# Kernel optimization log

Hardware: AMD Instinct MI355X
Metric: run time of the kernel (lower is better)

## Reference

```python
import jax, jax.numpy as jnp
import numpy as np

N_NODES = 50000
N_EDGES = 800000
N_FEATS = 64
K_HOPS = 3


def setup_inputs() -> dict:
    key = jax.random.key(0)
    k1, k2, k3 = jax.random.split(key, 3)
    x = jax.random.normal(k1, (N_NODES, N_FEATS), dtype=jnp.float32)
    edge_index = jax.random.randint(k2, (2, N_EDGES), 0, N_NODES, dtype=jnp.int32)
    # SGConv linear: out_channels = 1 (hardcoded in Net)
    W = jax.random.normal(k3, (1, N_FEATS), dtype=jnp.float32) / np.sqrt(N_FEATS)
    b = jnp.zeros((1,), dtype=jnp.float32)
    return {"x": x, "edge_index": edge_index, "W": W, "b": b}


def reference(x, edge_index, W, b):
    # SGConv: X' = (D^-1/2 (A + I) D^-1/2)^K X @ W.T + b
    N = x.shape[0]
    self_loops = jnp.arange(N, dtype=edge_index.dtype)
    row = jnp.concatenate([edge_index[0], self_loops])  # source nodes (x_j)
    col = jnp.concatenate([edge_index[1], self_loops])  # destination nodes
    # gcn_norm: degree computed at destination with unit edge weights
    deg = jax.ops.segment_sum(jnp.ones(row.shape[0], x.dtype), col, num_segments=N)
    dinv = jnp.where(deg > 0, jax.lax.rsqrt(deg), jnp.zeros_like(deg))
    norm = dinv[row] * dinv[col]  # [E + N]
    # K hops of normalized sparse propagation: out[col] += norm * x[row]
    for _ in range(K_HOPS):
        x = jax.ops.segment_sum(norm[:, None] * x[row], col, num_segments=N)
    return x @ W.T + b  # [N, 1]
```

## Files before the change

kernel.cpp:

```cpp
#include <hip/hip_runtime.h>

#define N_NODES 50000
#define N_EDGES 800000
#define N_FEATS 64
#define EB4     (N_EDGES / 4)
#define NBUCK   256
#define BRANGE  196
#define CAPB    4096
#define BZT     1024
#define PRT     512
#define HOPT    1024
#define MAXREC  (BZT * 4)

struct SmemSort { unsigned buf[MAXREC]; unsigned adr[MAXREC]; };


__global__ void __launch_bounds__(BZT) k_bucketize(
    const int* __restrict__ row, const int* __restrict__ col,
    int* __restrict__ gcur, unsigned* __restrict__ recs)
{
    __shared__ SmemSort u;
    __shared__ int s_cnt[NBUCK];
    __shared__ int s_off[NBUCK];
    __shared__ int s_wsum[4];
    __shared__ int s_total;

    const int t = threadIdx.x;
    if (t < NBUCK) s_cnt[t] = 0;
    __syncthreads();

    const int g = blockIdx.x * BZT + t;
    const bool valid = g < EB4;
    int4 c4, r4;
    int bk[4], rk[4];
    if (valid) {
        c4 = ((const int4*)col)[g];
        r4 = ((const int4*)row)[g];
        bk[0] = c4.x / BRANGE; rk[0] = atomicAdd(&s_cnt[bk[0]], 1);
        bk[1] = c4.y / BRANGE; rk[1] = atomicAdd(&s_cnt[bk[1]], 1);
        bk[2] = c4.z / BRANGE; rk[2] = atomicAdd(&s_cnt[bk[2]], 1);
        bk[3] = c4.w / BRANGE; rk[3] = atomicAdd(&s_cnt[bk[3]], 1);
    }
    __syncthreads();

    if (t < NBUCK) {
        const int lane = t & 63;
        const int cnt = s_cnt[t];
        int val = cnt;
        #pragma unroll
        for (int d = 1; d < 64; d <<= 1) {
            int tmp = __shfl_up(val, d);
            if (lane >= d) val += tmp;
        }
        if (lane == 63) s_wsum[t >> 6] = val;
        s_off[t] = val - cnt;
    }
    __syncthreads();
    if (t < NBUCK) {
        const int w4 = t >> 6;
        int base = 0;
        #pragma unroll
        for (int i = 0; i < 3; i++) if (i < w4) base += s_wsum[i];
        s_off[t] += base;
        const int cnt = s_cnt[t];
        s_cnt[t] = cnt ? atomicAdd(&gcur[t], cnt) : 0;
        if (t == 0) s_total = s_wsum[0] + s_wsum[1] + s_wsum[2] + s_wsum[3];
    }
    __syncthreads();

    if (valid) {
        const int cc[4] = {c4.x, c4.y, c4.z, c4.w};
        const int rr[4] = {r4.x, r4.y, r4.z, r4.w};
        #pragma unroll
        for (int i = 0; i < 4; i++) {
            const int b = bk[i];
            const int p = s_off[b] + rk[i];
            const int slot = s_cnt[b] + rk[i];
            u.buf[p] = ((unsigned)(cc[i] - b * BRANGE) << 16) | (unsigned)rr[i];
            u.adr[p] = (slot < CAPB) ? (unsigned)(b * CAPB + slot) : 0xFFFFFFFFu;
        }
    }
    __syncthreads();

    const int total = s_total;
    for (int p = t; p < total; p += BZT) {
        const unsigned a = u.adr[p];
        if (a != 0xFFFFFFFFu) recs[a] = u.buf[p];
    }
}

__global__ void __launch_bounds__(PRT) k_prep(
    const int* __restrict__ gcur, unsigned* __restrict__ recs,
    const float* __restrict__ x, const float* __restrict__ w,
    float* __restrict__ dinv, float* __restrict__ z0)
{
    __shared__ unsigned s_sorted[CAPB];
    __shared__ int s_deg[NBUCK];
    __shared__ int s_base[NBUCK];
    __shared__ int s_wsum[4];

    const int t = threadIdx.x;
    const int blk = blockIdx.x;
    if (t < NBUCK) s_deg[t] = 0;
    __syncthreads();

    const int sz = min(gcur[blk], CAPB);

    const uint2* rb2 = (const uint2*)(recs + (size_t)blk * CAPB);
    uint2 q[4];
    #pragma unroll
    for (int i = 0; i < 4; i++) {
        const int idx = t + i * PRT;
        q[i] = make_uint2(0u, 0u);
        if (2 * idx < sz) {
            q[i] = rb2[idx];
            atomicAdd(&s_deg[q[i].x >> 16], 1);
            if (2 * idx + 1 < sz) atomicAdd(&s_deg[q[i].y >> 16], 1);
        }
    }
    __syncthreads();

    if (t < NBUCK) {
        const int lane = t & 63;
        const int c = s_deg[t];
        int v = c;
        #pragma unroll
        for (int d = 1; d < 64; d <<= 1) {
            int tmp = __shfl_up(v, d);
            if (lane >= d) v += tmp;
        }
        if (lane == 63) s_wsum[t >> 6] = v;
        s_base[t] = v - c;
    }
    __syncthreads();
    if (t < NBUCK) {
        const int w4 = t >> 6;
        int base = 0;
        #pragma unroll
        for (int i = 0; i < 3; i++) if (i < w4) base += s_wsum[i];
        s_base[t] += base;
    }
    __syncthreads();

    #pragma unroll
    for (int i = 0; i < 4; i++) {
        const int idx = t + i * PRT;
        if (2 * idx < sz) {
            const int p0 = atomicAdd(&s_base[q[i].x >> 16], 1);
            s_sorted[p0] = q[i].x;
            if (2 * idx + 1 < sz) {
                const int p1 = atomicAdd(&s_base[q[i].y >> 16], 1);
                s_sorted[p1] = q[i].y;
            }
        }
    }
    __syncthreads();

    for (int p = t; p < sz; p += PRT)
        recs[(size_t)blk * CAPB + p] = s_sorted[p];

    if (t < BRANGE) {
        const int node = blk * BRANGE + t;
        if (node < N_NODES) {
            const float d = rsqrtf((float)(s_deg[t] + 1));
            dinv[node] = d;
            const float4* xr = (const float4*)(x + (size_t)node * N_FEATS);
            const float4* wr = (const float4*)w;
            float a = 0.0f;
            #pragma unroll
            for (int k = 0; k < N_FEATS / 4; k++) {
                const float4 v = xr[k];
                const float4 u = wr[k];
                a += v.x * u.x + v.y * u.y + v.z * u.z + v.w * u.w;
            }
            z0[node] = d * a;
        }
    }
}

template <bool FINAL>
__global__ void __launch_bounds__(HOPT) k_hop(
    const int* __restrict__ gcur, const unsigned* __restrict__ recs,
    const float* __restrict__ dinv, const float* __restrict__ zin,
    float* __restrict__ out, const float* __restrict__ bptr)
{
    __shared__ float s_acc[BRANGE];
    const int t = threadIdx.x;
    const int blk = blockIdx.x;
    if (t < BRANGE) s_acc[t] = 0.0f;
    __syncthreads();

    const int sz  = min(gcur[blk], CAPB);
    const int sz4 = sz >> 2;
    const uint4* rb4 = (const uint4*)(recs + (size_t)blk * CAPB);
    for (int e = t; e < sz4; e += HOPT) {
        const uint4 r = rb4[e];
        const float v0 = zin[r.x & 0xFFFFu];
        const float v1 = zin[r.y & 0xFFFFu];
        const float v2 = zin[r.z & 0xFFFFu];
        const float v3 = zin[r.w & 0xFFFFu];
        const unsigned d0 = r.x >> 16, d1 = r.y >> 16;
        const unsigned d2 = r.z >> 16, d3 = r.w >> 16;
        float s = v0;
        if (d1 == d0) s += v1; else { atomicAdd(&s_acc[d0], s); s = v1; }
        if (d2 == d1) s += v2; else { atomicAdd(&s_acc[d1], s); s = v2; }
        if (d3 == d2) s += v3; else { atomicAdd(&s_acc[d2], s); s = v3; }
        atomicAdd(&s_acc[d3], s);
    }
    if (t < (sz & 3)) {
        const unsigned r = recs[(size_t)blk * CAPB + (sz4 << 2) + t];
        atomicAdd(&s_acc[r >> 16], zin[r & 0xFFFFu]);
    }
    __syncthreads();

    if (t < BRANGE) {
        const int node = blk * BRANGE + t;
        if (node < N_NODES) {
            const float d = dinv[node];
            const float v = zin[node] + s_acc[t];
            out[node] = FINAL ? (d * v + bptr[0]) : (d * d * v);
        }
    }
}


extern "C" void kernel_launch(void* const* d_in, const int* in_sizes, int n_in,
                              void* d_out, int out_size, void* d_ws, size_t ws_size,
                              hipStream_t stream) {
    const float* x  = (const float*)d_in[0];
    const int*   ei = (const int*)d_in[1];
    const float* W  = (const float*)d_in[2];
    const float* b  = (const float*)d_in[3];
    float* out = (float*)d_out;

    const int* row = ei;
    const int* col = ei + N_EDGES;

    int*      gcur = (int*)d_ws;
    unsigned* recs = (unsigned*)(gcur + NBUCK);
    float*    dinv = (float*)(recs + (size_t)NBUCK * CAPB);
    float*    z0   = dinv + N_NODES;
    float*    z1   = z0 + N_NODES;

    hipMemsetAsync(gcur, 0, NBUCK * sizeof(int), stream);

    k_bucketize<<<(EB4 + BZT - 1) / BZT, BZT, 0, stream>>>(row, col, gcur, recs);
    k_prep<<<NBUCK, PRT, 0, stream>>>(gcur, recs, x, W, dinv, z0);
    k_hop<false><<<NBUCK, HOPT, 0, stream>>>(gcur, recs, dinv, z0, z1, nullptr);
    k_hop<false><<<NBUCK, HOPT, 0, stream>>>(gcur, recs, dinv, z1, z0, nullptr);
    k_hop<true ><<<NBUCK, HOPT, 0, stream>>>(gcur, recs, dinv, z0, out, b);
}
```

Before: 96.71 us.

## Replace shared-atomic scatter in hop kernels with CSR segmented gather reduction

The prep kernel now stores per-destination CSR offsets for each bucket. The hop kernels copy the bucket's sorted records into LDS, and four threads per destination node gather and sum source values, combining with shuffles. This removes the LDS atomic adds and the run-detection branches, and the block size is cut to 832 threads, about four lanes per node. In exchange it adds an LDS staging copy and load imbalance across nodes whose degrees differ.

```diff
diff --git a/kernel.cpp b/kernel.cpp
--- a/kernel.cpp
+++ b/kernel.cpp
@@ -9,8 +9,9 @@
 #define CAPB    4096
 #define BZT     1024
 #define PRT     512
-#define HOPT    1024
+#define HOPT    832
 #define MAXREC  (BZT * 4)
+#define OSTR    256
 
 struct SmemSort { unsigned buf[MAXREC]; unsigned adr[MAXREC]; };
 
@@ -92,7 +93,7 @@
 __global__ void __launch_bounds__(PRT) k_prep(
     const int* __restrict__ gcur, unsigned* __restrict__ recs,
     const float* __restrict__ x, const float* __restrict__ w,
-    float* __restrict__ dinv, float* __restrict__ z0)
+    int* __restrict__ offs, float* __restrict__ dinv, float* __restrict__ z0)
 {
     __shared__ unsigned s_sorted[CAPB];
     __shared__ int s_deg[NBUCK];
@@ -139,6 +140,7 @@
         #pragma unroll
         for (int i = 0; i < 3; i++) if (i < w4) base += s_wsum[i];
         s_base[t] += base;
+        if (t <= BRANGE) offs[blk * OSTR + t] = s_base[t];
     }
     __syncthreads();
 
@@ -181,43 +183,45 @@
 template <bool FINAL>
 __global__ void __launch_bounds__(HOPT) k_hop(
     const int* __restrict__ gcur, const unsigned* __restrict__ recs,
-    const float* __restrict__ dinv, const float* __restrict__ zin,
-    float* __restrict__ out, const float* __restrict__ bptr)
+    const int* __restrict__ offs, const float* __restrict__ dinv,
+    const float* __restrict__ zin, float* __restrict__ out,
+    const float* __restrict__ bptr)
 {
-    __shared__ float s_acc[BRANGE];
+    __shared__ unsigned rl[CAPB];
+    __shared__ int s_offs[BRANGE + 1];
+
     const int t = threadIdx.x;
     const int blk = blockIdx.x;
-    if (t < BRANGE) s_acc[t] = 0.0f;
-    __syncthreads();
-
     const int sz  = min(gcur[blk], CAPB);
-    const int sz4 = sz >> 2;
+    const int szw = (sz + 3) >> 2;
+
     const uint4* rb4 = (const uint4*)(recs + (size_t)blk * CAPB);
-    for (int e = t; e < sz4; e += HOPT) {
-        const uint4 r = rb4[e];
-        const float v0 = zin[r.x & 0xFFFFu];
-        const float v1 = zin[r.y & 0xFFFFu];
-        const float v2 = zin[r.z & 0xFFFFu];
-        const float v3 = zin[r.w & 0xFFFFu];
-        const unsigned d0 = r.x >> 16, d1 = r.y >> 16;
-        const unsigned d2 = r.z >> 16, d3 = r.w >> 16;
-        float s = v0;
-        if (d1 == d0) s += v1; else { atomicAdd(&s_acc[d0], s); s = v1; }
-        if (d2 == d1) s += v2; else { atomicAdd(&s_acc[d1], s); s = v2; }
-        if (d3 == d2) s += v3; else { atomicAdd(&s_acc[d2], s); s = v3; }
-        atomicAdd(&s_acc[d3], s);
-    }
-    if (t < (sz & 3)) {
-        const unsigned r = recs[(size_t)blk * CAPB + (sz4 << 2) + t];
-        atomicAdd(&s_acc[r >> 16], zin[r & 0xFFFFu]);
-    }
-    __syncthreads();
-
-    if (t < BRANGE) {
-        const int node = blk * BRANGE + t;
+    for (int e = t; e < szw; e += HOPT) ((uint4*)rl)[e] = rb4[e];
+    if (t <= BRANGE) s_offs[t] = offs[blk * OSTR + t];
+    __syncthreads();
+
+    float sum = 0.0f;
+    if (t < 4 * BRANGE) {
+        const int d = t >> 2;
+        const int j = t & 3;
+        const int e2 = s_offs[d + 1];
+        int k = s_offs[d] + j;
+        for (; k + 12 < e2; k += 16) {
+            const unsigned r0 = rl[k], r1 = rl[k + 4];
+            const unsigned r2 = rl[k + 8], r3 = rl[k + 12];
+            sum += zin[r0 & 0xFFFFu] + zin[r1 & 0xFFFFu]
+                 + zin[r2 & 0xFFFFu] + zin[r3 & 0xFFFFu];
+        }
+        for (; k < e2; k += 4) sum += zin[rl[k] & 0xFFFFu];
+    }
+    sum += __shfl_xor(sum, 1);
+    sum += __shfl_xor(sum, 2);
+
+    if (t < 4 * BRANGE && (t & 3) == 0) {
+        const int node = blk * BRANGE + (t >> 2);
         if (node < N_NODES) {
             const float d = dinv[node];
-            const float v = zin[node] + s_acc[t];
+            const float v = zin[node] + sum;
             out[node] = FINAL ? (d * v + bptr[0]) : (d * d * v);
         }
     }
@@ -238,15 +242,16 @@
 
     int*      gcur = (int*)d_ws;
     unsigned* recs = (unsigned*)(gcur + NBUCK);
-    float*    dinv = (float*)(recs + (size_t)NBUCK * CAPB);
+    int*      offs = (int*)(recs + (size_t)NBUCK * CAPB);
+    float*    dinv = (float*)(offs + NBUCK * OSTR);
     float*    z0   = dinv + N_NODES;
     float*    z1   = z0 + N_NODES;
 
     hipMemsetAsync(gcur, 0, NBUCK * sizeof(int), stream);
 
     k_bucketize<<<(EB4 + BZT - 1) / BZT, BZT, 0, stream>>>(row, col, gcur, recs);
-    k_prep<<<NBUCK, PRT, 0, stream>>>(gcur, recs, x, W, dinv, z0);
-    k_hop<false><<<NBUCK, HOPT, 0, stream>>>(gcur, recs, dinv, z0, z1, nullptr);
-    k_hop<false><<<NBUCK, HOPT, 0, stream>>>(gcur, recs, dinv, z1, z0, nullptr);
-    k_hop<true ><<<NBUCK, HOPT, 0, stream>>>(gcur, recs, dinv, z0, out, b);
-}
+    k_prep<<<NBUCK, PRT, 0, stream>>>(gcur, recs, x, W, offs, dinv, z0);
+    k_hop<false><<<NBUCK, HOPT, 0, stream>>>(gcur, recs, offs, dinv, z0, z1, nullptr);
+    k_hop<false><<<NBUCK, HOPT, 0, stream>>>(gcur, recs, offs, dinv, z1, z0, nullptr);
+    k_hop<true ><<<NBUCK, HOPT, 0, stream>>>(gcur, recs, offs, dinv, z0, out, b);
+}
```

Measured after the change: 99.68 us. 1.03x slower.

## Replace global atomic bucket cursors with per-block count/offset tables and gather

Applied to the files above, without the earlier changes.

Bucketize no longer reserves slots with global atomics on per-bucket cursors. Each block now writes its locally sorted records contiguously, plus a per-bucket count and offset table. The prep kernel scans these tables and gathers each bucket's pieces from all writer blocks into shared memory before sorting by destination. This removes the memset, the global atomic contention and the scattered writes, at the cost of an extra staging buffer and a strided gather in prep. It also raises the prep block size to 1024 threads.

```diff
diff --git a/kernel.cpp b/kernel.cpp
--- a/kernel.cpp
+++ b/kernel.cpp
@@ -5,31 +5,58 @@
 #define N_FEATS 64
 #define EB4     (N_EDGES / 4)
 #define NBUCK   256
+#define NWRIT   196
 #define BRANGE  196
 #define CAPB    4096
 #define BZT     1024
-#define PRT     512
+#define PRT     1024
 #define HOPT    1024
 #define MAXREC  (BZT * 4)
 
-struct SmemSort { unsigned buf[MAXREC]; unsigned adr[MAXREC]; };
-
+
+__device__ __forceinline__ void scan256(const int* cnt_in, int* base_out,
+                                        int* wsum, int* tot) {
+    const int t = threadIdx.x;
+    if (t < NBUCK) {
+        const int lane = t & 63;
+        const int c = cnt_in[t];
+        int v = c;
+        #pragma unroll
+        for (int d = 1; d < 64; d <<= 1) {
+            int tmp = __shfl_up(v, d);
+            if (lane >= d) v += tmp;
+        }
+        if (lane == 63) wsum[t >> 6] = v;
+        base_out[t] = v - c;
+    }
+    __syncthreads();
+    if (t < NBUCK) {
+        const int w4 = t >> 6;
+        int base = 0;
+        #pragma unroll
+        for (int i = 0; i < 3; i++) if (i < w4) base += wsum[i];
+        base_out[t] += base;
+        if (t == 0) *tot = wsum[0] + wsum[1] + wsum[2] + wsum[3];
+    }
+}
 
 __global__ void __launch_bounds__(BZT) k_bucketize(
     const int* __restrict__ row, const int* __restrict__ col,
-    int* __restrict__ gcur, unsigned* __restrict__ recs)
+    unsigned* __restrict__ cnt, unsigned* __restrict__ off2,
+    unsigned* __restrict__ recs2)
 {
-    __shared__ SmemSort u;
+    __shared__ unsigned sbuf[MAXREC];
     __shared__ int s_cnt[NBUCK];
     __shared__ int s_off[NBUCK];
     __shared__ int s_wsum[4];
     __shared__ int s_total;
 
     const int t = threadIdx.x;
+    const int blk = blockIdx.x;
     if (t < NBUCK) s_cnt[t] = 0;
     __syncthreads();
 
-    const int g = blockIdx.x * BZT + t;
+    const int g = blk * BZT + t;
     const bool valid = g < EB4;
     int4 c4, r4;
     int bk[4], rk[4];
@@ -43,30 +70,13 @@
     }
     __syncthreads();
 
-    if (t < NBUCK) {
-        const int lane = t & 63;
-        const int cnt = s_cnt[t];
-        int val = cnt;
-        #pragma unroll
-        for (int d = 1; d < 64; d <<= 1) {
-            int tmp = __shfl_up(val, d);
-            if (lane >= d) val += tmp;
-        }
-        if (lane == 63) s_wsum[t >> 6] = val;
-        s_off[t] = val - cnt;
-    }
-    __syncthreads();
-    if (t < NBUCK) {
-        const int w4 = t >> 6;
-        int base = 0;
-        #pragma unroll
-        for (int i = 0; i < 3; i++) if (i < w4) base += s_wsum[i];
-        s_off[t] += base;
-        const int cnt = s_cnt[t];
-        s_cnt[t] = cnt ? atomicAdd(&gcur[t], cnt) : 0;
-        if (t == 0) s_total = s_wsum[0] + s_wsum[1] + s_wsum[2] + s_wsum[3];
-    }
-    __syncthreads();
+    scan256(s_cnt, s_off, s_wsum, &s_total);
+    __syncthreads();
+
+    if (t < NBUCK) {
+        cnt[t * NBUCK + blk]  = (unsigned)s_cnt[t];
+        off2[t * NBUCK + blk] = (unsigned)s_off[t];
+    }
 
     if (valid) {
         const int cc[4] = {c4.x, c4.y, c4.z, c4.w};
@@ -74,90 +84,89 @@
         #pragma unroll
         for (int i = 0; i < 4; i++) {
             const int b = bk[i];
-            const int p = s_off[b] + rk[i];
-            const int slot = s_cnt[b] + rk[i];
-            u.buf[p] = ((unsigned)(cc[i] - b * BRANGE) << 16) | (unsigned)rr[i];
-            u.adr[p] = (slot < CAPB) ? (unsigned)(b * CAPB + slot) : 0xFFFFFFFFu;
+            sbuf[s_off[b] + rk[i]] =
+                ((unsigned)(cc[i] - b * BRANGE) << 16) | (unsigned)rr[i];
         }
     }
     __syncthreads();
 
     const int total = s_total;
-    for (int p = t; p < total; p += BZT) {
-        const unsigned a = u.adr[p];
-        if (a != 0xFFFFFFFFu) recs[a] = u.buf[p];
-    }
+    for (int p = t; p < total; p += BZT)
+        recs2[(size_t)blk * MAXREC + p] = sbuf[p];
 }
 
 __global__ void __launch_bounds__(PRT) k_prep(
-    const int* __restrict__ gcur, unsigned* __restrict__ recs,
-    const float* __restrict__ x, const float* __restrict__ w,
-    float* __restrict__ dinv, float* __restrict__ z0)
+    const unsigned* __restrict__ cnt, const unsigned* __restrict__ off2,
+    const unsigned* __restrict__ recs2, const float* __restrict__ x,
+    const float* __restrict__ w, unsigned* __restrict__ recs,
+    int* __restrict__ bsz, float* __restrict__ dinv, float* __restrict__ z0)
 {
+    __shared__ unsigned s_raw[CAPB];
     __shared__ unsigned s_sorted[CAPB];
+    __shared__ int s_rcnt[NBUCK];
+    __shared__ int s_roff[NBUCK];
+    __shared__ int s_rbase[NBUCK];
     __shared__ int s_deg[NBUCK];
-    __shared__ int s_base[NBUCK];
+    __shared__ int s_dbase[NBUCK];
     __shared__ int s_wsum[4];
+    __shared__ int s_tot;
 
     const int t = threadIdx.x;
     const int blk = blockIdx.x;
-    if (t < NBUCK) s_deg[t] = 0;
-    __syncthreads();
-
-    const int sz = min(gcur[blk], CAPB);
-
-    const uint2* rb2 = (const uint2*)(recs + (size_t)blk * CAPB);
-    uint2 q[4];
+
+    if (t < NBUCK) {
+        s_rcnt[t] = (t < NWRIT) ? (int)cnt[blk * NBUCK + t] : 0;
+        s_roff[t] = (t < NWRIT) ? (int)off2[blk * NBUCK + t] : 0;
+        s_deg[t] = 0;
+    }
+    __syncthreads();
+
+    scan256(s_rcnt, s_rbase, s_wsum, &s_tot);
+    __syncthreads();
+    const int sz = min(s_tot, CAPB);
+
+    if (t < 4 * NWRIT) {
+        const int gw = t >> 2;
+        const int j  = t & 3;
+        const int rc = s_rcnt[gw];
+        const int ro = s_roff[gw];
+        const int rb = s_rbase[gw];
+        const unsigned* src = recs2 + (size_t)gw * MAXREC + ro;
+        for (int i = j; i < rc; i += 4) {
+            const int pos = rb + i;
+            if (pos < CAPB) s_raw[pos] = src[i];
+        }
+    }
+    __syncthreads();
+
+    unsigned q[4];
     #pragma unroll
     for (int i = 0; i < 4; i++) {
         const int idx = t + i * PRT;
-        q[i] = make_uint2(0u, 0u);
-        if (2 * idx < sz) {
-            q[i] = rb2[idx];
-            atomicAdd(&s_deg[q[i].x >> 16], 1);
-            if (2 * idx + 1 < sz) atomicAdd(&s_deg[q[i].y >> 16], 1);
-        }
-    }
-    __syncthreads();
-
-    if (t < NBUCK) {
-        const int lane = t & 63;
-        const int c = s_deg[t];
-        int v = c;
-        #pragma unroll
-        for (int d = 1; d < 64; d <<= 1) {
-            int tmp = __shfl_up(v, d);
-            if (lane >= d) v += tmp;
-        }
-        if (lane == 63) s_wsum[t >> 6] = v;
-        s_base[t] = v - c;
-    }
-    __syncthreads();
-    if (t < NBUCK) {
-        const int w4 = t >> 6;
-        int base = 0;
-        #pragma unroll
-        for (int i = 0; i < 3; i++) if (i < w4) base += s_wsum[i];
-        s_base[t] += base;
-    }
+        q[i] = 0u;
+        if (idx < sz) {
+            q[i] = s_raw[idx];
+            atomicAdd(&s_deg[q[i] >> 16], 1);
+        }
+    }
+    __syncthreads();
+
+    scan256(s_deg, s_dbase, s_wsum, &s_tot);
     __syncthreads();
 
     #pragma unroll
     for (int i = 0; i < 4; i++) {
         const int idx = t + i * PRT;
-        if (2 * idx < sz) {
-            const int p0 = atomicAdd(&s_base[q[i].x >> 16], 1);
-            s_sorted[p0] = q[i].x;
-            if (2 * idx + 1 < sz) {
-                const int p1 = atomicAdd(&s_base[q[i].y >> 16], 1);
-                s_sorted[p1] = q[i].y;
-            }
+        if (idx < sz) {
+            const int p = atomicAdd(&s_dbase[q[i] >> 16], 1);
+            s_sorted[p] = q[i];
         }
     }
     __syncthreads();
 
     for (int p = t; p < sz; p += PRT)
         recs[(size_t)blk * CAPB + p] = s_sorted[p];
+    if (t == 0) bsz[blk] = sz;
 
     if (t < BRANGE) {
         const int node = blk * BRANGE + t;
@@ -180,7 +189,7 @@
 
 template <bool FINAL>
 __global__ void __launch_bounds__(HOPT) k_hop(
-    const int* __restrict__ gcur, const unsigned* __restrict__ recs,
+    const int* __restrict__ bsz, const unsigned* __restrict__ recs,
     const float* __restrict__ dinv, const float* __restrict__ zin,
     float* __restrict__ out, const float* __restrict__ bptr)
 {
@@ -190,7 +199,7 @@
     if (t < BRANGE) s_acc[t] = 0.0f;
     __syncthreads();
 
-    const int sz  = min(gcur[blk], CAPB);
+    const int sz  = min(bsz[blk], CAPB);
     const int sz4 = sz >> 2;
     const uint4* rb4 = (const uint4*)(recs + (size_t)blk * CAPB);
     for (int e = t; e < sz4; e += HOPT) {
@@ -236,17 +245,18 @@
     const int* row = ei;
     const int* col = ei + N_EDGES;
 
-    int*      gcur = (int*)d_ws;
-    unsigned* recs = (unsigned*)(gcur + NBUCK);
-    float*    dinv = (float*)(recs + (size_t)NBUCK * CAPB);
-    float*    z0   = dinv + N_NODES;
-    float*    z1   = z0 + N_NODES;
-
-    hipMemsetAsync(gcur, 0, NBUCK * sizeof(int), stream);
-
-    k_bucketize<<<(EB4 + BZT - 1) / BZT, BZT, 0, stream>>>(row, col, gcur, recs);
-    k_prep<<<NBUCK, PRT, 0, stream>>>(gcur, recs, x, W, dinv, z0);
-    k_hop<false><<<NBUCK, HOPT, 0, stream>>>(gcur, recs, dinv, z0, z1, nullptr);
-    k_hop<false><<<NBUCK, HOPT, 0, stream>>>(gcur, recs, dinv, z1, z0, nullptr);
-    k_hop<true ><<<NBUCK, HOPT, 0, stream>>>(gcur, recs, dinv, z0, out, b);
-}
+    unsigned* cnt   = (unsigned*)d_ws;
+    unsigned* off2  = cnt + NBUCK * NBUCK;
+    unsigned* recs2 = off2 + NBUCK * NBUCK;
+    unsigned* recs  = recs2 + (size_t)NBUCK * MAXREC;
+    int*      bsz   = (int*)(recs + (size_t)NBUCK * CAPB);
+    float*    dinv  = (float*)(bsz + NBUCK);
+    float*    z0    = dinv + N_NODES;
+    float*    z1    = z0 + N_NODES;
+
+    k_bucketize<<<NWRIT, BZT, 0, stream>>>(row, col, cnt, off2, recs2);
+    k_prep<<<NBUCK, PRT, 0, stream>>>(cnt, off2, recs2, x, W, recs, bsz, dinv, z0);
+    k_hop<false><<<NBUCK, HOPT, 0, stream>>>(bsz, recs, dinv, z0, z1, nullptr);
+    k_hop<false><<<NBUCK, HOPT, 0, stream>>>(bsz, recs, dinv, z1, z0, nullptr);
+    k_hop<true ><<<NBUCK, HOPT, 0, stream>>>(bsz, recs, dinv, z0, out, b);
+}
```

After: 95.82 us. About the same (-0.9%).
